# Kernel optimization log

Hardware: AMD Instinct MI355X
Metric: run time of the kernel (lower is better)

## Reference

```python
import jax, jax.numpy as jnp
import numpy as np

N_LAYERS = 4
D_MODEL = 256
P = 128            # ssm_size // 2 (conj_sym S5)
LATENT_DIM = 256
MAX_SEQ_LEN = 32768
OUTPUT_DIM = 64
LN_EPS = 1e-6      # flax nn.LayerNorm default


def layer_norm(x, scale, bias):
    mu = jnp.mean(x, axis=-1, keepdims=True)
    var = jnp.mean(jnp.square(x - mu), axis=-1, keepdims=True)
    return (x - mu) * jax.lax.rsqrt(var + LN_EPS) * scale + bias


def s5_ssm(u, Lre, Lim, Bre, Bim, Cre, Cim, Dvec, log_step, resets):
    """u: (L, H) float. Returns (L, H) float. conj_sym S5, zoh discretization."""
    step = jnp.exp(log_step)                       # (P,)
    Lam = Lre + 1j * Lim                           # (P,) complex
    Lam_bar = jnp.exp(Lam * step)                  # (P,)
    B_bar = ((Lam_bar - 1.0) / Lam)[:, None] * (Bre + 1j * Bim)  # (P, H)
    Bu = u @ B_bar.T                               # (L, P) complex
    A = jnp.broadcast_to(Lam_bar, Bu.shape)        # (L, P)
    c = resets[:, None].astype(u.dtype)            # (L, 1)

    def binop(qi, qj):
        Ai, bi, ci = qi
        Aj, bj, cj = qj
        return (Aj * Ai * (1.0 - cj) + Aj * cj,
                (Aj * bi + bj) * (1.0 - cj) + bj * cj,
                ci * (1.0 - cj) + cj)

    # zero initial hidden state => no prepend needed (identical result)
    _, xs, _ = jax.lax.associative_scan(binop, (A, Bu, c))
    y = 2.0 * jnp.real(xs @ (Cre + 1j * Cim).T)    # (L, H), conj_sym doubling
    return y + u * Dvec


def setup_inputs() -> dict:
    key = jax.random.key(0)
    ks = jax.random.split(key, 16)
    f = jax.random.normal
    return {
        "latent": f(ks[0], (LATENT_DIM,), jnp.float32),
        "W_expand": f(ks[1], (LATENT_DIM, D_MODEL), jnp.float32) / np.sqrt(LATENT_DIM),
        "b_expand": jnp.zeros((D_MODEL,), jnp.float32),
        "norm_scale": jnp.ones((N_LAYERS, D_MODEL), jnp.float32),
        "norm_bias": jnp.zeros((N_LAYERS, D_MODEL), jnp.float32),
        "Lambda_re": -(0.1 + 0.9 * jax.random.uniform(ks[2], (N_LAYERS, P))),
        "Lambda_im": np.pi * f(ks[3], (N_LAYERS, P), jnp.float32),
        "B_re": f(ks[4], (N_LAYERS, P, D_MODEL), jnp.float32) / np.sqrt(D_MODEL),
        "B_im": f(ks[5], (N_LAYERS, P, D_MODEL), jnp.float32) / np.sqrt(D_MODEL),
        "C_re": f(ks[6], (N_LAYERS, D_MODEL, P), jnp.float32) / np.sqrt(P),
        "C_im": f(ks[7], (N_LAYERS, D_MODEL, P), jnp.float32) / np.sqrt(P),
        "D": f(ks[8], (N_LAYERS, D_MODEL), jnp.float32),
        "log_step": jnp.log(jax.random.uniform(ks[9], (N_LAYERS, P), minval=1e-3, maxval=1e-1)),
        "W1": f(ks[10], (N_LAYERS, D_MODEL, D_MODEL), jnp.float32) / np.sqrt(D_MODEL),
        "b1": jnp.zeros((N_LAYERS, D_MODEL), jnp.float32),
        "W2": f(ks[11], (N_LAYERS, D_MODEL, D_MODEL), jnp.float32) / np.sqrt(D_MODEL),
        "b2": jnp.zeros((N_LAYERS, D_MODEL), jnp.float32),
        "W_out": f(ks[12], (D_MODEL, OUTPUT_DIM), jnp.float32) / np.sqrt(D_MODEL),
        "b_out": jnp.zeros((OUTPUT_DIM,), jnp.float32),
        "seq_len": MAX_SEQ_LEN,
    }


def reference(latent, W_expand, b_expand, norm_scale, norm_bias,
              Lambda_re, Lambda_im, B_re, B_im, C_re, C_im, D, log_step,
              W1, b1, W2, b2, W_out, b_out, seq_len):
    # latent_expand + leaky_relu, then broadcast to full trajectory
    x = jax.nn.leaky_relu(latent @ W_expand + b_expand)        # (H,)
    x = jnp.broadcast_to(x[None, :], (MAX_SEQ_LEN, D_MODEL))    # (L, H); batch dim of 1 dropped
    resets = jnp.zeros((MAX_SEQ_LEN,), x.dtype)                 # dones = zeros
    for i in range(N_LAYERS):
        skip = x
        h = layer_norm(x, norm_scale[i], norm_bias[i])          # prenorm
        y = s5_ssm(h, Lambda_re[i], Lambda_im[i], B_re[i], B_im[i],
                   C_re[i], C_im[i], D[i], log_step[i], resets)
        y = layer_norm(y, norm_scale[i], norm_bias[i])          # gtrxl norm (shared params)
        y = jax.nn.gelu(y)
        y = (y @ W1[i] + b1[i]) * jax.nn.sigmoid(y @ W2[i] + b2[i])  # full_glu
        x = skip + y
    return x @ W_out + b_out                                    # (L, output_dim)
```

## Files before the change

kernel.cpp:

```cpp
#include <hip/hip_runtime.h>
#include <stdint.h>

#define LSEQ 32768
#define NCH 512
#define TCH 64

typedef _Float16 half8 __attribute__((ext_vector_type(8)));
typedef _Float16 half4v __attribute__((ext_vector_type(4)));
typedef _Float16 half2v __attribute__((ext_vector_type(2)));
typedef float f32x4 __attribute__((ext_vector_type(4)));
typedef float f32x2 __attribute__((ext_vector_type(2)));

__device__ __forceinline__ float sigmoidf_(float x) { return 1.f / (1.f + __expf(-x)); }
__device__ __forceinline__ float gelu_(float x) {
    float z = 0.7978845608028654f * (x + 0.044715f * x * x * x);
    float e = __expf(2.f * z);
    float t = 1.f - 2.f / (e + 1.f);
    return 0.5f * x * (1.f + t);
}

__device__ __forceinline__ void gll16(const _Float16* gp, _Float16* lp) {
    __builtin_amdgcn_global_load_lds((__attribute__((address_space(1))) void*)gp,
                                     (__attribute__((address_space(3))) void*)lp, 16, 0, 0);
}

template <int BM, int BN, int BK, int WR, int WC>
__device__ __forceinline__ void gemm_core(const _Float16* __restrict__ A,
                                          const _Float16* __restrict__ Wt,
                                          _Float16* sA, _Float16* sW,
                                          int m0, int n0,
                                          f32x4 (&acc)[BM / (WR * 16)][BN / (WC * 16)]) {
    constexpr int MT = BM / (WR * 16);
    constexpr int NT = BN / (WC * 16);
    constexpr int KS = BK / 32;
    constexpr int CA = KS * (BM / 16);
    constexpr int CW = KS * (BN / 16);
    constexpr int NKB = 256 / BK;
    constexpr int NWAVE = WR * WC;
    const int tid = threadIdx.x;
    const int wid = tid >> 6;
    const int lane = tid & 63;
    const int wm = wid / WC;
    const int wn = wid % WC;

    f32x4 zero = {0.f, 0.f, 0.f, 0.f};
#pragma unroll
    for (int i = 0; i < MT; ++i)
#pragma unroll
        for (int j = 0; j < NT; ++j) acc[i][j] = zero;

    auto stage = [&](int kb, int buf) {
#pragma unroll
        for (int i = 0; i < CA / NWAVE; ++i) {
            int c = i * NWAVE + wid;
            int ks = c / (BM / 16), r16 = c % (BM / 16);
            const _Float16* gp = A + (m0 + r16 * 16 + (lane & 15)) * 256 + kb + ks * 32 + (lane >> 4) * 8;
            gll16(gp, sA + buf * (CA * 512) + c * 512);
        }
#pragma unroll
        for (int i = 0; i < CW / NWAVE; ++i) {
            int c = i * NWAVE + wid;
            int ks = c / (BN / 16), n16 = c % (BN / 16);
            const _Float16* gp = Wt + (n0 + n16 * 16 + (lane & 15)) * 256 + kb + ks * 32 + (lane >> 4) * 8;
            gll16(gp, sW + buf * (CW * 512) + c * 512);
        }
    };

    stage(0, 0);
#pragma unroll
    for (int t = 0; t < NKB; ++t) {
        __syncthreads();
        if (t + 1 < NKB) stage((t + 1) * BK, (t + 1) & 1);
        const _Float16* bA = sA + (t & 1) * (CA * 512);
        const _Float16* bW = sW + (t & 1) * (CW * 512);
#pragma unroll
        for (int ks = 0; ks < KS; ++ks) {
            half8 af[MT], bf[NT];
#pragma unroll
            for (int mt = 0; mt < MT; ++mt)
                af[mt] = *(const half8*)(bA + (ks * (BM / 16) + wm * MT + mt) * 512 + lane * 8);
#pragma unroll
            for (int nt = 0; nt < NT; ++nt)
                bf[nt] = *(const half8*)(bW + (ks * (BN / 16) + wn * NT + nt) * 512 + lane * 8);
#pragma unroll
            for (int mt = 0; mt < MT; ++mt)
#pragma unroll
                for (int nt = 0; nt < NT; ++nt)
                    acc[mt][nt] = __builtin_amdgcn_mfma_f32_16x16x32_f16(af[mt], bf[nt], acc[mt][nt], 0, 0, 0);
        }
    }
    __syncthreads();
}

__global__ __launch_bounds__(512) void s5_k0a(const float* __restrict__ lre, const float* __restrict__ lim,
                                              const float* __restrict__ lstep,
                                              float* aR, float* aI, float* cbR, float* cbI,
                                              float* aTR, float* aTI, float* alp, float* ralp) {
    int i = threadIdx.x;
    float st = expf(lstep[i]);
    float lr = lre[i] * st, li = lim[i] * st;
    float ea = expf(lr);
    float ar = ea * cosf(li), ai = ea * sinf(li);
    float den = lre[i] * lre[i] + lim[i] * lim[i];
    float nr = ar - 1.f, ni = ai;
    float cr = (nr * lre[i] + ni * lim[i]) / den;
    float ci = (ni * lre[i] - nr * lim[i]) / den;
    float cm = sqrtf(cr * cr + ci * ci);
    float al = sqrtf(2.83f / fmaxf(cm, 1e-8f));
    float eT = expf(lr * (float)TCH);
    aR[i] = ar; aI[i] = ai;
    cbR[i] = cr; cbI[i] = ci;
    aTR[i] = eT * cosf(li * (float)TCH);
    aTI[i] = eT * sinf(li * (float)TCH);
    alp[i] = al; ralp[i] = 1.f / al;
}

__global__ __launch_bounds__(256) void s5_k0b(const float* __restrict__ Bre, const float* __restrict__ Bim,
                                              const float* __restrict__ Cre, const float* __restrict__ Cim,
                                              const float* __restrict__ W1, const float* __restrict__ W2,
                                              const float* __restrict__ b1, const float* __restrict__ b2,
                                              const float* __restrict__ Wout,
                                              const float* __restrict__ cbR, const float* __restrict__ cbI,
                                              const float* __restrict__ alp, const float* __restrict__ ralp,
                                              _Float16* Wbu, _Float16* Wc, _Float16* Wglu,
                                              _Float16* WoutT, float* bglu) {
    int stride = gridDim.x * blockDim.x;
    int tid0 = blockIdx.x * blockDim.x + threadIdx.x;
    for (int i = tid0; i < 262144; i += stride) {
        int l = i >> 16, n = (i >> 8) & 255, k = i & 255;
        int s = n >> 4, lmn = n & 15;
        int p = l * 128 + (s >> 1) * 16 + lmn;
        float re = cbR[p] * Bre[p * 256 + k] - cbI[p] * Bim[p * 256 + k];
        float im = cbR[p] * Bim[p * 256 + k] + cbI[p] * Bre[p * 256 + k];
        Wbu[i] = (_Float16)(((s & 1) ? im : re) * alp[p]);
    }
    for (int i = tid0; i < 262144; i += stride) {
        int l = i >> 16, n = (i >> 8) & 255, k = i & 255;
        int p = k >> 1;
        float base = (k & 1) ? -2.f * Cim[(l * 256 + n) * 128 + p]
                             : 2.f * Cre[(l * 256 + n) * 128 + p];
        Wc[i] = (_Float16)(base * ralp[l * 128 + p]);
    }
    for (int i = tid0; i < 524288; i += stride) {
        int l = i >> 17, n = (i >> 8) & 511, k = i & 255;
        int j = ((n >> 7) << 6) | (((n >> 6) & 1) << 5) | (((n >> 5) & 1) << 4) | (n & 15);
        const float* src = ((n >> 4) & 1) ? W2 : W1;
        Wglu[i] = (_Float16)src[(l * 256 + k) * 256 + j];
    }
    for (int i = tid0; i < 16384; i += stride) {
        int n = i >> 8, k = i & 255;
        WoutT[i] = (_Float16)Wout[k * 64 + n];
    }
    for (int i = tid0; i < 2048; i += stride) {
        int l = i >> 9, n = i & 511;
        int j = ((n >> 7) << 6) | (((n >> 6) & 1) << 5) | (((n >> 5) & 1) << 4) | (n & 15);
        bglu[i] = (((n >> 4) & 1) ? b2 : b1)[l * 256 + j];
    }
}

__global__ __launch_bounds__(256) void s5_k0c(const float* __restrict__ latent, const float* __restrict__ W,
                                              const float* __restrict__ b, _Float16* __restrict__ x0h) {
    __shared__ float lat[256];
    lat[threadIdx.x] = latent[threadIdx.x];
    __syncthreads();
    float s = b[threadIdx.x];
    for (int k = 0; k < 256; ++k) s += lat[k] * W[k * 256 + threadIdx.x];
    x0h[threadIdx.x] = (_Float16)((s > 0.f) ? s : 0.01f * s);
}

__global__ __launch_bounds__(256) void s5_k1_fill(const _Float16* __restrict__ x0h, _Float16* __restrict__ x) {
    int i = blockIdx.x * 256 + threadIdx.x;
    half8 v = *(const half8*)(x0h + (i & 31) * 8);
    *(half8*)(x + i * 8) = v;
}

__global__ __launch_bounds__(512, 2) void s5_k3_lngemm(const _Float16* __restrict__ x,
                                                       const _Float16* __restrict__ Wt,
                                                       const float* __restrict__ gamma,
                                                       const float* __restrict__ beta,
                                                       _Float16* __restrict__ h,
                                                       _Float16* __restrict__ Buh) {
    __shared__ _Float16 sW[64 * 512];
    int tid = threadIdx.x, wid = tid >> 6, lane = tid & 63;
    int lm = lane & 15, quad = lane >> 4;
    int m0 = blockIdx.x * 128;
    int rowb = m0 + wid * 16;

    auto stageW = [&](int half) {
#pragma unroll
        for (int i = 0; i < 8; ++i) {
            int c = i * 8 + wid;
            int ks = c >> 3, n16 = c & 7;
            gll16(Wt + (half * 128 + n16 * 16 + lm) * 256 + ks * 32 + quad * 8, sW + c * 512);
        }
    };
    stageW(0);

    int row = rowb + lm;
    half8 af[8];
    {
        half8 xv[8];
#pragma unroll
        for (int ks = 0; ks < 8; ++ks)
            xv[ks] = *(const half8*)(x + row * 256 + ks * 32 + quad * 8);
        float s1 = 0.f, s2 = 0.f;
#pragma unroll
        for (int i = 0; i < 8; ++i)
#pragma unroll
            for (int j = 0; j < 8; ++j) { float t = (float)xv[i][j]; s1 += t; s2 += t * t; }
        s1 += __shfl_xor(s1, 16, 64); s2 += __shfl_xor(s2, 16, 64);
        s1 += __shfl_xor(s1, 32, 64); s2 += __shfl_xor(s2, 32, 64);
        float mu = s1 * (1.f / 256.f);
        float var = s2 * (1.f / 256.f) - mu * mu;
        float rs = rsqrtf(fmaxf(var, 0.f) + 1e-6f);
#pragma unroll
        for (int ks = 0; ks < 8; ++ks) {
            f32x4 g0 = *(const f32x4*)(gamma + ks * 32 + quad * 8);
            f32x4 g1 = *(const f32x4*)(gamma + ks * 32 + quad * 8 + 4);
            f32x4 b0 = *(const f32x4*)(beta + ks * 32 + quad * 8);
            f32x4 b1 = *(const f32x4*)(beta + ks * 32 + quad * 8 + 4);
            half8 o;
#pragma unroll
            for (int j = 0; j < 4; ++j) {
                o[j]     = (_Float16)(((float)xv[ks][j] - mu) * rs * g0[j] + b0[j]);
                o[j + 4] = (_Float16)(((float)xv[ks][j + 4] - mu) * rs * g1[j] + b1[j]);
            }
            af[ks] = o;
            *(half8*)(h + row * 256 + ks * 32 + quad * 8) = o;
        }
    }
    asm volatile("s_waitcnt vmcnt(0)" ::: "memory");
    __syncthreads();

    f32x4 zero = {0.f, 0.f, 0.f, 0.f};
    f32x4 acc[2][8];
#pragma unroll
    for (int hf = 0; hf < 2; ++hf)
#pragma unroll
        for (int nt = 0; nt < 8; ++nt) acc[hf][nt] = zero;

#pragma unroll
    for (int ks = 0; ks < 8; ++ks) {
        half8 bf[8];
#pragma unroll
        for (int nt = 0; nt < 8; ++nt)
            bf[nt] = *(const half8*)(sW + (ks * 8 + nt) * 512 + lane * 8);
#pragma unroll
        for (int nt = 0; nt < 8; ++nt)
            acc[0][nt] = __builtin_amdgcn_mfma_f32_16x16x32_f16(af[ks], bf[nt], acc[0][nt], 0, 0, 0);
    }
    __syncthreads();
    stageW(1);
    asm volatile("s_waitcnt vmcnt(0)" ::: "memory");
    __syncthreads();
#pragma unroll
    for (int ks = 0; ks < 8; ++ks) {
        half8 bf[8];
#pragma unroll
        for (int nt = 0; nt < 8; ++nt)
            bf[nt] = *(const half8*)(sW + (ks * 8 + nt) * 512 + lane * 8);
#pragma unroll
        for (int nt = 0; nt < 8; ++nt)
            acc[1][nt] = __builtin_amdgcn_mfma_f32_16x16x32_f16(af[ks], bf[nt], acc[1][nt], 0, 0, 0);
    }

#pragma unroll
    for (int u = 0; u < 8; ++u) {
        int hf = u >> 2, q = u & 3;
        int p = u * 16 + lm;
#pragma unroll
        for (int r = 0; r < 4; ++r) {
            half2v o = {(_Float16)acc[hf][2 * q][r], (_Float16)acc[hf][2 * q + 1][r]};
            *(half2v*)(Buh + (rowb + quad * 4 + r) * 256 + 2 * p) = o;
        }
    }
}

__global__ __launch_bounds__(128, 4) void s5_k4_carry(const _Float16* __restrict__ Bu,
                                                      const float* __restrict__ aR, const float* __restrict__ aI,
                                                      float* __restrict__ carRI) {
    int p = threadIdx.x, c = blockIdx.x;
    int t0 = c * TCH;
    const _Float16* bp = Bu + t0 * 256 + 2 * p;
    half2v hv[TCH];
#pragma unroll
    for (int j = 0; j < TCH; ++j) hv[j] = *(const half2v*)(bp + j * 256);
    float ar = aR[p], ai = aI[p];
    float sr = 0.f, si = 0.f;
#pragma unroll
    for (int j = 0; j < TCH; ++j) {
        float nr = fmaf(ar, sr, fmaf(-ai, si, (float)hv[j][0]));
        float ni = fmaf(ar, si, fmaf(ai, sr, (float)hv[j][1]));
        sr = nr; si = ni;
    }
    *(f32x2*)(carRI + (c * 128 + p) * 2) = f32x2{sr, si};
}

__global__ __launch_bounds__(128, 4) void s5_k6_scan(const _Float16* __restrict__ Bu,
                                                     const float* __restrict__ carRI,
                                                     const float* __restrict__ aR, const float* __restrict__ aI,
                                                     const float* __restrict__ aTR, const float* __restrict__ aTI,
                                                     _Float16* __restrict__ xs2) {
    int p = threadIdx.x, c = blockIdx.x;
    int t0 = c * TCH;
    const _Float16* bp = Bu + t0 * 256 + 2 * p;
    half2v hv[TCH];
#pragma unroll
    for (int j = 0; j < TCH; ++j) hv[j] = *(const half2v*)(bp + j * 256);
    float tr = aTR[p], ti = aTI[p];
    float cr = 0.f, ci = 0.f;
#pragma unroll 8
    for (int i = 0; i < c; ++i) {
        f32x2 w = *(const f32x2*)(carRI + (i * 128 + p) * 2);
        float nr = fmaf(tr, cr, fmaf(-ti, ci, w[0]));
        float ni = fmaf(tr, ci, fmaf(ti, cr, w[1]));
        cr = nr; ci = ni;
    }
    float ar = aR[p], ai = aI[p];
    float sr = cr, si = ci;
    _Float16* op = xs2 + t0 * 256 + 2 * p;
#pragma unroll
    for (int j = 0; j < TCH; ++j) {
        float nr = fmaf(ar, sr, fmaf(-ai, si, (float)hv[j][0]));
        float ni = fmaf(ar, si, fmaf(ai, sr, (float)hv[j][1]));
        sr = nr; si = ni;
        *(half2v*)(op + j * 256) = half2v{(_Float16)sr, (_Float16)si};
    }
}

__global__ __launch_bounds__(512, 2) void s5_k7_gemm_c(const _Float16* __restrict__ A,
                                                       const _Float16* __restrict__ Wt,
                                                       const _Float16* __restrict__ h,
                                                       const float* __restrict__ Dv,
                                                       const float* __restrict__ gamma,
                                                       const float* __restrict__ beta,
                                                       _Float16* __restrict__ g) {
    __shared__ _Float16 sW[64 * 512];
    int tid = threadIdx.x, wid = tid >> 6, lane = tid & 63;
    int lm = lane & 15, quad = lane >> 4;
    int m0 = blockIdx.x * 128;
    int rowb = m0 + wid * 16;

    auto stageW = [&](int half) {
#pragma unroll
        for (int i = 0; i < 8; ++i) {
            int c = i * 8 + wid;
            int ks = c >> 3, n16 = c & 7;
            gll16(Wt + (half * 128 + n16 * 16 + lm) * 256 + ks * 32 + quad * 8, sW + c * 512);
        }
    };
    stageW(0);
    half8 af[8];
#pragma unroll
    for (int ks = 0; ks < 8; ++ks)
        af[ks] = *(const half8*)(A + (rowb + lm) * 256 + ks * 32 + quad * 8);
    asm volatile("s_waitcnt vmcnt(0)" ::: "memory");
    __syncthreads();

    f32x4 zero = {0.f, 0.f, 0.f, 0.f};
    f32x4 acc[2][8];
#pragma unroll
    for (int hf = 0; hf < 2; ++hf)
#pragma unroll
        for (int nt = 0; nt < 8; ++nt) acc[hf][nt] = zero;

#pragma unroll
    for (int ks = 0; ks < 8; ++ks) {
        half8 bf[8];
#pragma unroll
        for (int nt = 0; nt < 8; ++nt)
            bf[nt] = *(const half8*)(sW + (ks * 8 + nt) * 512 + lane * 8);
#pragma unroll
        for (int nt = 0; nt < 8; ++nt)
            acc[0][nt] = __builtin_amdgcn_mfma_f32_16x16x32_f16(af[ks], bf[nt], acc[0][nt], 0, 0, 0);
    }
    __syncthreads();
    stageW(1);
    asm volatile("s_waitcnt vmcnt(0)" ::: "memory");
    __syncthreads();
#pragma unroll
    for (int ks = 0; ks < 8; ++ks) {
        half8 bf[8];
#pragma unroll
        for (int nt = 0; nt < 8; ++nt)
            bf[nt] = *(const half8*)(sW + (ks * 8 + nt) * 512 + lane * 8);
#pragma unroll
        for (int nt = 0; nt < 8; ++nt)
            acc[1][nt] = __builtin_amdgcn_mfma_f32_16x16x32_f16(af[ks], bf[nt], acc[1][nt], 0, 0, 0);
    }

#pragma unroll
    for (int hf = 0; hf < 2; ++hf)
#pragma unroll
        for (int nt = 0; nt < 8; ++nt) {
            int col = hf * 128 + nt * 16 + lm;
            float dv = Dv[col];
#pragma unroll
            for (int r = 0; r < 4; ++r)
                acc[hf][nt][r] += (float)h[(rowb + quad * 4 + r) * 256 + col] * dv;
        }
    float mu[4], rs[4];
#pragma unroll
    for (int r = 0; r < 4; ++r) {
        float a = 0.f, b = 0.f;
#pragma unroll
        for (int hf = 0; hf < 2; ++hf)
#pragma unroll
            for (int nt = 0; nt < 8; ++nt) {
                float v = acc[hf][nt][r];
                a += v; b += v * v;
            }
#pragma unroll
        for (int off = 1; off < 16; off <<= 1) {
            a += __shfl_xor(a, off, 64);
            b += __shfl_xor(b, off, 64);
        }
        float m = a * (1.f / 256.f);
        float var = b * (1.f / 256.f) - m * m;
        mu[r] = m;
        rs[r] = rsqrtf(fmaxf(var, 0.f) + 1e-6f);
    }
#pragma unroll
    for (int hf = 0; hf < 2; ++hf)
#pragma unroll
        for (int nt = 0; nt < 8; ++nt) {
            int col = hf * 128 + nt * 16 + lm;
            float ga = gamma[col], be = beta[col];
#pragma unroll
            for (int r = 0; r < 4; ++r) {
                float hn = (acc[hf][nt][r] - mu[r]) * rs[r] * ga + be;
                g[(rowb + quad * 4 + r) * 256 + col] = (_Float16)gelu_(hn);
            }
        }
}

__global__ __launch_bounds__(256, 2) void s5_k8_gemm_glu(const _Float16* __restrict__ A,
                                                         const _Float16* __restrict__ Wt,
                                                         const float* __restrict__ bias,
                                                         _Float16* __restrict__ x) {
    __shared__ _Float16 sW[64 * 512];
    int tid = threadIdx.x, wid = tid >> 6, lane = tid & 63;
    int lm = lane & 15, quad = lane >> 4;
    int n0 = blockIdx.y * 128;
    int m0 = blockIdx.x * 128;
#pragma unroll
    for (int i = 0; i < 16; ++i) {
        int c = i * 4 + wid;
        int ks = c >> 3, n16 = c & 7;
        gll16(Wt + (n0 + n16 * 16 + lm) * 256 + ks * 32 + quad * 8, sW + c * 512);
    }
    int rowb = m0 + wid * 32;
    half8 af[2][8];
#pragma unroll
    for (int mt = 0; mt < 2; ++mt)
#pragma unroll
        for (int ks = 0; ks < 8; ++ks)
            af[mt][ks] = *(const half8*)(A + (rowb + mt * 16 + lm) * 256 + ks * 32 + quad * 8);
    asm volatile("s_waitcnt vmcnt(0)" ::: "memory");
    __syncthreads();

    f32x4 zero = {0.f, 0.f, 0.f, 0.f};
    f32x4 acc[2][8];
#pragma unroll
    for (int mt = 0; mt < 2; ++mt)
#pragma unroll
        for (int nt = 0; nt < 8; ++nt) acc[mt][nt] = zero;
#pragma unroll
    for (int ks = 0; ks < 8; ++ks) {
        half8 bf[8];
#pragma unroll
        for (int nt = 0; nt < 8; ++nt)
            bf[nt] = *(const half8*)(sW + (ks * 8 + nt) * 512 + lane * 8);
#pragma unroll
        for (int mt = 0; mt < 2; ++mt)
#pragma unroll
            for (int nt = 0; nt < 8; ++nt)
                acc[mt][nt] = __builtin_amdgcn_mfma_f32_16x16x32_f16(af[mt][ks], bf[nt], acc[mt][nt], 0, 0, 0);
    }
    int jbase = (n0 >> 1) + lm;
    _Float16 xold[2][4][4];
#pragma unroll
    for (int mt = 0; mt < 2; ++mt)
#pragma unroll
        for (int q = 0; q < 4; ++q)
#pragma unroll
            for (int r = 0; r < 4; ++r)
                xold[mt][q][r] = x[(rowb + mt * 16 + quad * 4 + r) * 256 + jbase + q * 16];
#pragma unroll
    for (int mt = 0; mt < 2; ++mt)
#pragma unroll
        for (int q = 0; q < 4; ++q) {
            float b1v = bias[n0 + (2 * q) * 16 + lm];
            float b2v = bias[n0 + (2 * q + 1) * 16 + lm];
            int jcol = jbase + q * 16;
#pragma unroll
            for (int r = 0; r < 4; ++r) {
                float u1 = acc[mt][2 * q][r] + b1v;
                float u2 = acc[mt][2 * q + 1][r] + b2v;
                float gl = u1 * sigmoidf_(u2);
                int idx = (rowb + mt * 16 + quad * 4 + r) * 256 + jcol;
                x[idx] = (_Float16)((float)xold[mt][q][r] + gl);
            }
        }
}

__global__ __launch_bounds__(256) void s5_k9_gemm_out(const _Float16* __restrict__ A,
                                                      const _Float16* __restrict__ Wt,
                                                      const float* __restrict__ bout,
                                                      float* __restrict__ out) {
    __shared__ _Float16 sA[2 * 16 * 512], sW[2 * 8 * 512];
    f32x4 acc[2][4];
    int m0 = blockIdx.x * 128;
    gemm_core<128, 64, 64, 4, 1>(A, Wt, sA, sW, m0, 0, acc);
    int tid = threadIdx.x, wid = tid >> 6, lane = tid & 63, lm = lane & 15, quad = lane >> 4;
#pragma unroll
    for (int mt = 0; mt < 2; ++mt)
#pragma unroll
        for (int nt = 0; nt < 4; ++nt) {
            int col = nt * 16 + lm;
            float bv = bout[col];
#pragma unroll
            for (int r = 0; r < 4; ++r) {
                int row = m0 + wid * 32 + mt * 16 + quad * 4 + r;
                out[row * 64 + col] = acc[mt][nt][r] + bv;
            }
        }
}

constexpr size_t OFF_X    = 0;
constexpr size_t OFF_BU   = 33554432;
constexpr size_t OFF_H    = 67108864;
constexpr size_t OFF_WBU  = 100663296;
constexpr size_t OFF_WC   = OFF_WBU + 524288;
constexpr size_t OFF_WGLU = OFF_WC + 524288;
constexpr size_t OFF_WOUT = OFF_WGLU + 1048576;
constexpr size_t OFF_BGLU = OFF_WOUT + 32768;
constexpr size_t OFF_AR   = OFF_BGLU + 8192;
constexpr size_t OFF_AI   = OFF_AR + 2048;
constexpr size_t OFF_CBR  = OFF_AI + 2048;
constexpr size_t OFF_CBI  = OFF_CBR + 2048;
constexpr size_t OFF_ATR  = OFF_CBI + 2048;
constexpr size_t OFF_ATI  = OFF_ATR + 2048;
constexpr size_t OFF_ALP  = OFF_ATI + 2048;
constexpr size_t OFF_RALP = OFF_ALP + 2048;
constexpr size_t OFF_X0H  = OFF_RALP + 2048;
constexpr size_t OFF_CARRI= OFF_X0H + 1024;

extern "C" void kernel_launch(void* const* d_in, const int* in_sizes, int n_in,
                              void* d_out, int out_size, void* d_ws, size_t ws_size,
                              hipStream_t stream) {
    (void)in_sizes; (void)n_in; (void)out_size; (void)ws_size;
    const float* latent    = (const float*)d_in[0];
    const float* W_expand  = (const float*)d_in[1];
    const float* b_expand  = (const float*)d_in[2];
    const float* norm_s    = (const float*)d_in[3];
    const float* norm_b    = (const float*)d_in[4];
    const float* Lre       = (const float*)d_in[5];
    const float* Lim       = (const float*)d_in[6];
    const float* Bre       = (const float*)d_in[7];
    const float* Bim       = (const float*)d_in[8];
    const float* Cre       = (const float*)d_in[9];
    const float* Cim       = (const float*)d_in[10];
    const float* Dv        = (const float*)d_in[11];
    const float* lstep     = (const float*)d_in[12];
    const float* W1        = (const float*)d_in[13];
    const float* b1        = (const float*)d_in[14];
    const float* W2        = (const float*)d_in[15];
    const float* b2        = (const float*)d_in[16];
    const float* Wout      = (const float*)d_in[17];
    const float* bout      = (const float*)d_in[18];

    char* ws = (char*)d_ws;
    _Float16* x    = (_Float16*)(ws + OFF_X);
    _Float16* Buh  = (_Float16*)(ws + OFF_BU);
    _Float16* xs2  = (_Float16*)(ws + OFF_BU);
    _Float16* gbuf = (_Float16*)(ws + OFF_BU + 16777216);
    _Float16* hbuf = (_Float16*)(ws + OFF_H);
    _Float16* Wbu  = (_Float16*)(ws + OFF_WBU);
    _Float16* Wc   = (_Float16*)(ws + OFF_WC);
    _Float16* Wglu = (_Float16*)(ws + OFF_WGLU);
    _Float16* WoutT= (_Float16*)(ws + OFF_WOUT);
    float* bglu = (float*)(ws + OFF_BGLU);
    float* aR  = (float*)(ws + OFF_AR);
    float* aI  = (float*)(ws + OFF_AI);
    float* cbR = (float*)(ws + OFF_CBR);
    float* cbI = (float*)(ws + OFF_CBI);
    float* aTR = (float*)(ws + OFF_ATR);
    float* aTI = (float*)(ws + OFF_ATI);
    float* alp = (float*)(ws + OFF_ALP);
    float* ralp= (float*)(ws + OFF_RALP);
    _Float16* x0h = (_Float16*)(ws + OFF_X0H);
    float* carRI=(float*)(ws + OFF_CARRI);

    s5_k0a<<<1, 512, 0, stream>>>(Lre, Lim, lstep, aR, aI, cbR, cbI, aTR, aTI, alp, ralp);
    s5_k0b<<<256, 256, 0, stream>>>(Bre, Bim, Cre, Cim, W1, W2, b1, b2, Wout,
                                    cbR, cbI, alp, ralp, Wbu, Wc, Wglu, WoutT, bglu);
    s5_k0c<<<1, 256, 0, stream>>>(latent, W_expand, b_expand, x0h);
    s5_k1_fill<<<4096, 256, 0, stream>>>(x0h, x);

    for (int l = 0; l < 4; ++l) {
        s5_k3_lngemm<<<256, 512, 0, stream>>>(x, Wbu + l * 65536,
                                              norm_s + l * 256, norm_b + l * 256,
                                              hbuf, Buh);
        s5_k4_carry<<<NCH, 128, 0, stream>>>(Buh, aR + l * 128, aI + l * 128, carRI);
        s5_k6_scan<<<NCH, 128, 0, stream>>>(Buh, carRI, aR + l * 128, aI + l * 128,
                                            aTR + l * 128, aTI + l * 128, xs2);
        s5_k7_gemm_c<<<256, 512, 0, stream>>>(xs2, Wc + l * 65536, hbuf, Dv + l * 256,
                                              norm_s + l * 256, norm_b + l * 256, gbuf);
        s5_k8_gemm_glu<<<dim3(256, 4), 256, 0, stream>>>(gbuf, Wglu + l * 131072,
                                                         bglu + l * 512, x);
    }
    s5_k9_gemm_out<<<256, 256, 0, stream>>>(x, WoutT, bout, (float*)d_out);
}
```

Measured before the change: 512.1 us.

## Fuse carry and scan into one cooperative kernel with grid sync

Merges the chunk-carry kernel and the chunk-scan kernel into a single cooperative launch. A grid-wide barrier separates the carry computation from the carry propagation and output pass, so the Bu values stay in registers and are not loaded twice. It also halves the chunk length and doubles the chunk count. The cost is a grid sync, a serial carry-propagation loop that is now up to twice as long, and a cooperative launch that needs all blocks resident at once. It also relies on the precomputed chunk-power coefficients following the new TCH.

New measurement: 965.6 us. +88.6%, slower.

```diff
diff --git a/kernel.cpp b/kernel.cpp
--- a/kernel.cpp
+++ b/kernel.cpp
@@ -1,9 +1,12 @@
 #include <hip/hip_runtime.h>
+#include <hip/hip_cooperative_groups.h>
 #include <stdint.h>
 
+namespace cg = cooperative_groups;
+
 #define LSEQ 32768
-#define NCH 512
-#define TCH 64
+#define NCH 1024
+#define TCH 32
 
 typedef _Float16 half8 __attribute__((ext_vector_type(8)));
 typedef _Float16 half4v __attribute__((ext_vector_type(4)));
@@ -276,9 +279,11 @@
     }
 }
 
-__global__ __launch_bounds__(128, 4) void s5_k4_carry(const _Float16* __restrict__ Bu,
+__global__ __launch_bounds__(128, 4) void s5_k46_scan(const _Float16* __restrict__ Bu,
                                                       const float* __restrict__ aR, const float* __restrict__ aI,
-                                                      float* __restrict__ carRI) {
+                                                      const float* __restrict__ aTR, const float* __restrict__ aTI,
+                                                      float* __restrict__ carRI,
+                                                      _Float16* __restrict__ xs2) {
     int p = threadIdx.x, c = blockIdx.x;
     int t0 = c * TCH;
     const _Float16* bp = Bu + t0 * 256 + 2 * p;
@@ -294,19 +299,9 @@
         sr = nr; si = ni;
     }
     *(f32x2*)(carRI + (c * 128 + p) * 2) = f32x2{sr, si};
-}
-
-__global__ __launch_bounds__(128, 4) void s5_k6_scan(const _Float16* __restrict__ Bu,
-                                                     const float* __restrict__ carRI,
-                                                     const float* __restrict__ aR, const float* __restrict__ aI,
-                                                     const float* __restrict__ aTR, const float* __restrict__ aTI,
-                                                     _Float16* __restrict__ xs2) {
-    int p = threadIdx.x, c = blockIdx.x;
-    int t0 = c * TCH;
-    const _Float16* bp = Bu + t0 * 256 + 2 * p;
-    half2v hv[TCH];
-#pragma unroll
-    for (int j = 0; j < TCH; ++j) hv[j] = *(const half2v*)(bp + j * 256);
+
+    cg::this_grid().sync();
+
     float tr = aTR[p], ti = aTI[p];
     float cr = 0.f, ci = 0.f;
 #pragma unroll 8
@@ -316,15 +311,14 @@
         float ni = fmaf(tr, ci, fmaf(ti, cr, w[1]));
         cr = nr; ci = ni;
     }
-    float ar = aR[p], ai = aI[p];
-    float sr = cr, si = ci;
+    float s2r = cr, s2i = ci;
     _Float16* op = xs2 + t0 * 256 + 2 * p;
 #pragma unroll
     for (int j = 0; j < TCH; ++j) {
-        float nr = fmaf(ar, sr, fmaf(-ai, si, (float)hv[j][0]));
-        float ni = fmaf(ar, si, fmaf(ai, sr, (float)hv[j][1]));
-        sr = nr; si = ni;
-        *(half2v*)(op + j * 256) = half2v{(_Float16)sr, (_Float16)si};
+        float nr = fmaf(ar, s2r, fmaf(-ai, s2i, (float)hv[j][0]));
+        float ni = fmaf(ar, s2i, fmaf(ai, s2r, (float)hv[j][1]));
+        s2r = nr; s2i = ni;
+        *(half2v*)(op + j * 256) = half2v{(_Float16)s2r, (_Float16)s2i};
     }
 }
 
@@ -602,9 +596,18 @@
         s5_k3_lngemm<<<256, 512, 0, stream>>>(x, Wbu + l * 65536,
                                               norm_s + l * 256, norm_b + l * 256,
                                               hbuf, Buh);
-        s5_k4_carry<<<NCH, 128, 0, stream>>>(Buh, aR + l * 128, aI + l * 128, carRI);
-        s5_k6_scan<<<NCH, 128, 0, stream>>>(Buh, carRI, aR + l * 128, aI + l * 128,
-                                            aTR + l * 128, aTI + l * 128, xs2);
+        {
+            const _Float16* buArg = Buh;
+            const float* aRl  = aR + l * 128;
+            const float* aIl  = aI + l * 128;
+            const float* aTRl = aTR + l * 128;
+            const float* aTIl = aTI + l * 128;
+            float* carArg = carRI;
+            _Float16* xsArg = xs2;
+            void* args[] = {&buArg, &aRl, &aIl, &aTRl, &aTIl, &carArg, &xsArg};
+            hipLaunchCooperativeKernel((const void*)s5_k46_scan, dim3(NCH), dim3(128),
+                                       args, 0, stream);
+        }
         s5_k7_gemm_c<<<256, 512, 0, stream>>>(xs2, Wc + l * 65536, hbuf, Dv + l * 256,
                                               norm_s + l * 256, norm_b + l * 256, gbuf);
         s5_k8_gemm_glu<<<dim3(256, 4), 256, 0, stream>>>(gbuf, Wglu + l * 131072,
```
